# Kernel optimization log

Measured on AMD Instinct MI355X. Metric: run time of the kernel, lower is better.

Reference implementation:

```python
import jax, jax.numpy as jnp
import numpy as np

NUM_TOKENS = 131072
N_EXPERTS = 256
N_GROUP = 8
TOPK_GROUP = 4
TOP_K = 8
ROUTED_SCALING = 2.5


def setup_inputs() -> dict:
    key = jax.random.key(0)
    k1, k2 = jax.random.split(key)
    router_logits = jax.random.normal(k1, (NUM_TOKENS, N_EXPERTS), dtype=jnp.float32)
    correction_bias = jax.random.normal(k2, (N_EXPERTS,), dtype=jnp.float32) * 0.1
    return {"router_logits": router_logits, "correction_bias": correction_bias}


def reference(router_logits, correction_bias):
    T = router_logits.shape[0]
    eg = N_EXPERTS // N_GROUP  # experts per group = 32

    scores = jax.nn.sigmoid(router_logits).astype(jnp.float32)          # [T, 256]
    scores_for_choice = scores + correction_bias[None, :]                # [T, 256]

    # group score = sum of top-2 corrected scores within each group
    grp = scores_for_choice.reshape(T, N_GROUP, eg)                      # [T, 8, 32]
    top2, _ = jax.lax.top_k(grp, 2)                                      # [T, 8, 2]
    group_scores = top2.sum(axis=-1)                                     # [T, 8]

    # pick top groups, build expert-level mask
    _, group_idx = jax.lax.top_k(group_scores, TOPK_GROUP)               # [T, 4]
    rows = jnp.arange(T)[:, None]
    group_mask = jnp.zeros_like(group_scores).at[rows, group_idx].set(1.0)  # [T, 8]
    score_mask = jnp.repeat(group_mask, eg, axis=-1)                     # [T, 256]

    masked_scores = jnp.where(score_mask > 0, scores_for_choice, 0.0)
    _, topk_indices = jax.lax.top_k(masked_scores, TOP_K)                # [T, 8]

    topk_weights = jnp.take_along_axis(scores, topk_indices, axis=1)     # [T, 8]
    denom = topk_weights.sum(axis=-1, keepdims=True) + 1e-20
    topk_weights = topk_weights / denom * ROUTED_SCALING
    return (topk_indices, topk_weights)
```

## Files before the change

kernel.cpp:

```cpp
#include <hip/hip_runtime.h>
#include <math.h>


constexpr int N_EXPERTS   = 256;
constexpr int N_GROUP     = 8;
constexpr int EG          = 32;
constexpr int TOPK_GROUP  = 4;
constexpr int TOP_K       = 8;
constexpr int BLOCK       = 256;

__device__ __forceinline__ void insert8(float (&lv)[8], float (&li)[8], float v, float i) {
#pragma unroll
  for (int k = 0; k < 8; ++k) {
    const bool gt = v > lv[k];
    const float nv = gt ? lv[k] : v;
    const float ni = gt ? li[k] : i;
    lv[k] = gt ? v : lv[k];
    li[k] = gt ? i : li[k];
    v = nv; i = ni;
  }
}

__device__ __forceinline__ bool keyGE(float va, float ia, float vb, float ib) {
  return (va > vb) || (va == vb && ia < ib);
}

__device__ __forceinline__ void takeMax(float va, float ia, float vb, float ib,
                                        float& vo, float& io) {
  const bool a = keyGE(va, ia, vb, ib);
  vo = a ? va : vb;
  io = a ? ia : ib;
}

__device__ __forceinline__ void cswap(float& va, float& ia, float& vb, float& ib) {
  const bool a = keyGE(va, ia, vb, ib);
  const float v1 = a ? va : vb, i1 = a ? ia : ib;
  const float v2 = a ? vb : va, i2 = a ? ib : ia;
  va = v1; ia = i1; vb = v2; ib = i2;
}

__device__ __forceinline__ void merge8(const float (&Av)[8], const float (&Ai)[8],
                                       const float (&Bv)[8], const float (&Bi)[8],
                                       float (&Rv)[8], float (&Ri)[8]) {
#pragma unroll
  for (int i = 0; i < 8; ++i) takeMax(Av[i], Ai[i], Bv[7 - i], Bi[7 - i], Rv[i], Ri[i]);
#pragma unroll
  for (int i = 0; i < 4; ++i) cswap(Rv[i], Ri[i], Rv[i + 4], Ri[i + 4]);
  cswap(Rv[0], Ri[0], Rv[2], Ri[2]);
  cswap(Rv[1], Ri[1], Rv[3], Ri[3]);
  cswap(Rv[4], Ri[4], Rv[6], Ri[6]);
  cswap(Rv[5], Ri[5], Rv[7], Ri[7]);
  cswap(Rv[0], Ri[0], Rv[1], Ri[1]);
  cswap(Rv[2], Ri[2], Rv[3], Ri[3]);
  cswap(Rv[4], Ri[4], Rv[5], Ri[5]);
  cswap(Rv[6], Ri[6], Rv[7], Ri[7]);
}

__global__ __launch_bounds__(256, 2) void deepseek_topk_router_lds(
    const float* __restrict__ logits,
    const float* __restrict__ bias,
    float* __restrict__ out,
    int T) {
  __shared__ float gsbuf[BLOCK];
  __shared__ float exv[8 * BLOCK];
  __shared__ float exi[8 * BLOCK];

  const int tid = threadIdx.x;
  const int id  = blockIdx.x * BLOCK + tid;
  const int t   = id >> 3;
  const int q   = id & 7;

  const float4* row4 =
      reinterpret_cast<const float4*>(logits + (size_t)t * N_EXPERTS + q * EG);
  const float4* b4 = reinterpret_cast<const float4*>(bias + q * EG);

  float lv[8], li[8];
#pragma unroll
  for (int k = 0; k < 8; ++k) { lv[k] = -INFINITY; li[k] = 0.0f; }

#pragma unroll
  for (int u = 0; u < 8; ++u) {
    const float4 x = row4[u];
    const float4 bb = b4[u];
    const float xs[4] = {x.x, x.y, x.z, x.w};
    const float bs[4] = {bb.x, bb.y, bb.z, bb.w};
#pragma unroll
    for (int e = 0; e < 4; ++e) {
      const int idx = q * EG + u * 4 + e;
      const float s = 1.0f / (1.0f + expf(-xs[e]));
      const float c = s + bs[e];
      insert8(lv, li, c, (float)idx);
    }
  }

  const float gs = lv[0] + lv[1];
  gsbuf[tid] = gs;
  __syncthreads();
  const int cbase = tid & ~7;
  int rank = 0;
#pragma unroll
  for (int h = 0; h < N_GROUP; ++h) {
    const float other = gsbuf[cbase + h];
    rank += ((other > gs) || (other == gs && h < q)) ? 1 : 0;
  }
  const bool sel = (rank < TOPK_GROUP);
#pragma unroll
  for (int k = 0; k < 8; ++k) lv[k] = sel ? lv[k] : 0.0f;

  float pv[8], pi[8], rv[8], ri[8];
#pragma unroll
  for (int d = 1; d <= 4; d <<= 1) {
    __syncthreads();
#pragma unroll
    for (int k = 0; k < 8; ++k) {
      exv[k * BLOCK + tid] = lv[k];
      exi[k * BLOCK + tid] = li[k];
    }
    __syncthreads();
    const int p = tid ^ d;
#pragma unroll
    for (int k = 0; k < 8; ++k) {
      pv[k] = exv[k * BLOCK + p];
      pi[k] = exi[k * BLOCK + p];
    }
    merge8(lv, li, pv, pi, rv, ri);
#pragma unroll
    for (int k = 0; k < 8; ++k) { lv[k] = rv[k]; li[k] = ri[k]; }
  }

  float sv[8];
  float sum = 0.0f;
#pragma unroll
  for (int k = 0; k < TOP_K; ++k) {
    const int idf = (int)li[k];
    sv[k] = lv[k] - bias[idf];
    sum += sv[k];
  }
  const float scale = 2.5f / (sum + 1e-20f);

  if (q < 4) {
    float4 vout;
    if (q == 0)      vout = make_float4(li[0], li[1], li[2], li[3]);
    else if (q == 1) vout = make_float4(li[4], li[5], li[6], li[7]);
    else if (q == 2) vout = make_float4(sv[0] * scale, sv[1] * scale,
                                        sv[2] * scale, sv[3] * scale);
    else             vout = make_float4(sv[4] * scale, sv[5] * scale,
                                        sv[6] * scale, sv[7] * scale);
    const size_t half = (q < 2) ? 0 : (size_t)T * TOP_K;
    const int    sub  = q & 1;
    float4* dst = reinterpret_cast<float4*>(out + half) + (size_t)t * 2 + sub;
    *dst = vout;
  }
}

extern "C" void kernel_launch(void* const* d_in, const int* in_sizes, int n_in,
                              void* d_out, int out_size, void* d_ws, size_t ws_size,
                              hipStream_t stream) {
  const float* logits = (const float*)d_in[0];
  const float* bias   = (const float*)d_in[1];
  float* out = (float*)d_out;
  const int T = in_sizes[0] / N_EXPERTS;
  const long threads = (long)T * N_GROUP;
  const int blocks = (int)((threads + BLOCK - 1) / BLOCK);
  deepseek_topk_router_lds<<<blocks, BLOCK, 0, stream>>>(logits, bias, out, T);
}
```

Baseline: 217.8 us.

## Replace insertion top-8 and butterfly exchange with sort-merge and single LDS gather

The per-group top-8 is now built by sorting 8-element chunks with an odd-even network and merging them, replacing 32 serial insertions. After one barrier, each thread computes the four selected group indices directly and gathers those groups' sorted lists from LDS with vector loads, then merges them. This removes the three-round butterfly exchange and its six extra barriers. Launch bounds now request 4 blocks per CU. The tradeoffs are more redundant merge work per thread and higher register pressure, plus possible changes in tie-breaking order.

```diff
diff --git a/kernel.cpp b/kernel.cpp
--- a/kernel.cpp
+++ b/kernel.cpp
@@ -2,22 +2,25 @@
 #include <math.h>
 
 
-constexpr int N_EXPERTS   = 256;
-constexpr int N_GROUP     = 8;
-constexpr int EG          = 32;
-constexpr int TOPK_GROUP  = 4;
-constexpr int TOP_K       = 8;
-constexpr int BLOCK       = 256;
-
-__device__ __forceinline__ void insert8(float (&lv)[8], float (&li)[8], float v, float i) {
-#pragma unroll
-  for (int k = 0; k < 8; ++k) {
-    const bool gt = v > lv[k];
-    const float nv = gt ? lv[k] : v;
-    const float ni = gt ? li[k] : i;
-    lv[k] = gt ? v : lv[k];
-    li[k] = gt ? i : li[k];
-    v = nv; i = ni;
+constexpr int N_EXPERTS  = 256;
+constexpr int N_GROUP    = 8;
+constexpr int EG         = 32;
+constexpr int TOPK_GROUP = 4;
+constexpr int TOP_K      = 8;
+constexpr int BLOCK      = 256;
+
+__device__ __forceinline__ void sort8_stable(float (&v)[8], float (&i)[8]) {
+#pragma unroll
+  for (int r = 0; r < 8; ++r) {
+#pragma unroll
+    for (int k = (r & 1); k + 1 < 8; k += 2) {
+      const bool sw = v[k + 1] > v[k];
+      const float tv = sw ? v[k + 1] : v[k];
+      const float bv = sw ? v[k]     : v[k + 1];
+      const float ti = sw ? i[k + 1] : i[k];
+      const float bi = sw ? i[k]     : i[k + 1];
+      v[k] = tv; v[k + 1] = bv; i[k] = ti; i[k + 1] = bi;
+    }
   }
 }
 
@@ -25,45 +28,44 @@
   return (va > vb) || (va == vb && ia < ib);
 }
 
-__device__ __forceinline__ void takeMax(float va, float ia, float vb, float ib,
-                                        float& vo, float& io) {
-  const bool a = keyGE(va, ia, vb, ib);
-  vo = a ? va : vb;
-  io = a ? ia : ib;
-}
-
-__device__ __forceinline__ void cswap(float& va, float& ia, float& vb, float& ib) {
+__device__ __forceinline__ void cswapKey(float& va, float& ia, float& vb, float& ib) {
   const bool a = keyGE(va, ia, vb, ib);
   const float v1 = a ? va : vb, i1 = a ? ia : ib;
   const float v2 = a ? vb : va, i2 = a ? ib : ia;
   va = v1; ia = i1; vb = v2; ib = i2;
 }
 
-__device__ __forceinline__ void merge8(const float (&Av)[8], const float (&Ai)[8],
-                                       const float (&Bv)[8], const float (&Bi)[8],
-                                       float (&Rv)[8], float (&Ri)[8]) {
-#pragma unroll
-  for (int i = 0; i < 8; ++i) takeMax(Av[i], Ai[i], Bv[7 - i], Bi[7 - i], Rv[i], Ri[i]);
-#pragma unroll
-  for (int i = 0; i < 4; ++i) cswap(Rv[i], Ri[i], Rv[i + 4], Ri[i + 4]);
-  cswap(Rv[0], Ri[0], Rv[2], Ri[2]);
-  cswap(Rv[1], Ri[1], Rv[3], Ri[3]);
-  cswap(Rv[4], Ri[4], Rv[6], Ri[6]);
-  cswap(Rv[5], Ri[5], Rv[7], Ri[7]);
-  cswap(Rv[0], Ri[0], Rv[1], Ri[1]);
-  cswap(Rv[2], Ri[2], Rv[3], Ri[3]);
-  cswap(Rv[4], Ri[4], Rv[5], Ri[5]);
-  cswap(Rv[6], Ri[6], Rv[7], Ri[7]);
-}
-
-__global__ __launch_bounds__(256, 2) void deepseek_topk_router_lds(
+__device__ __forceinline__ void merge8AB(float (&Av)[8], float (&Ai)[8],
+                                         const float (&Bv)[8], const float (&Bi)[8]) {
+  float Rv[8], Ri[8];
+#pragma unroll
+  for (int i = 0; i < 8; ++i) {
+    const bool a = (Av[i] >= Bv[7 - i]);
+    Rv[i] = a ? Av[i] : Bv[7 - i];
+    Ri[i] = a ? Ai[i] : Bi[7 - i];
+  }
+#pragma unroll
+  for (int i = 0; i < 4; ++i) cswapKey(Rv[i], Ri[i], Rv[i + 4], Ri[i + 4]);
+  cswapKey(Rv[0], Ri[0], Rv[2], Ri[2]);
+  cswapKey(Rv[1], Ri[1], Rv[3], Ri[3]);
+  cswapKey(Rv[4], Ri[4], Rv[6], Ri[6]);
+  cswapKey(Rv[5], Ri[5], Rv[7], Ri[7]);
+  cswapKey(Rv[0], Ri[0], Rv[1], Ri[1]);
+  cswapKey(Rv[2], Ri[2], Rv[3], Ri[3]);
+  cswapKey(Rv[4], Ri[4], Rv[5], Ri[5]);
+  cswapKey(Rv[6], Ri[6], Rv[7], Ri[7]);
+#pragma unroll
+  for (int i = 0; i < 8; ++i) { Av[i] = Rv[i]; Ai[i] = Ri[i]; }
+}
+
+__global__ __launch_bounds__(256, 4) void deepseek_topk_router_r6(
     const float* __restrict__ logits,
     const float* __restrict__ bias,
     float* __restrict__ out,
     int T) {
-  __shared__ float gsbuf[BLOCK];
-  __shared__ float exv[8 * BLOCK];
-  __shared__ float exi[8 * BLOCK];
+  __shared__ float gsb[BLOCK];
+  __shared__ __align__(16) float exv[BLOCK * 8];
+  __shared__ __align__(16) float exi[BLOCK * 8];
 
   const int tid = threadIdx.x;
   const int id  = blockIdx.x * BLOCK + tid;
@@ -73,75 +75,113 @@
   const float4* row4 =
       reinterpret_cast<const float4*>(logits + (size_t)t * N_EXPERTS + q * EG);
   const float4* b4 = reinterpret_cast<const float4*>(bias + q * EG);
-
-  float lv[8], li[8];
-#pragma unroll
-  for (int k = 0; k < 8; ++k) { lv[k] = -INFINITY; li[k] = 0.0f; }
-
-#pragma unroll
-  for (int u = 0; u < 8; ++u) {
-    const float4 x = row4[u];
-    const float4 bb = b4[u];
-    const float xs[4] = {x.x, x.y, x.z, x.w};
-    const float bs[4] = {bb.x, bb.y, bb.z, bb.w};
-#pragma unroll
-    for (int e = 0; e < 4; ++e) {
-      const int idx = q * EG + u * 4 + e;
-      const float s = 1.0f / (1.0f + expf(-xs[e]));
-      const float c = s + bs[e];
-      insert8(lv, li, c, (float)idx);
+  const float basef = (float)(q * EG);
+
+  float Tv[8], Ti[8];
+  {
+    const float4 x0 = row4[0], x1 = row4[1];
+    const float4 c0 = b4[0],   c1 = b4[1];
+    const float xs[8] = {x0.x, x0.y, x0.z, x0.w, x1.x, x1.y, x1.z, x1.w};
+    const float bs[8] = {c0.x, c0.y, c0.z, c0.w, c1.x, c1.y, c1.z, c1.w};
+#pragma unroll
+    for (int j = 0; j < 8; ++j) {
+      Tv[j] = 1.0f / (1.0f + expf(-xs[j])) + bs[j];
+      Ti[j] = basef + (float)j;
     }
-  }
-
-  const float gs = lv[0] + lv[1];
-  gsbuf[tid] = gs;
+    sort8_stable(Tv, Ti);
+  }
+#pragma unroll
+  for (int c = 1; c < 4; ++c) {
+    float Cv[8], Ci[8];
+    const float4 x0 = row4[2 * c], x1 = row4[2 * c + 1];
+    const float4 c0 = b4[2 * c],   c1 = b4[2 * c + 1];
+    const float xs[8] = {x0.x, x0.y, x0.z, x0.w, x1.x, x1.y, x1.z, x1.w};
+    const float bs[8] = {c0.x, c0.y, c0.z, c0.w, c1.x, c1.y, c1.z, c1.w};
+#pragma unroll
+    for (int j = 0; j < 8; ++j) {
+      Cv[j] = 1.0f / (1.0f + expf(-xs[j])) + bs[j];
+      Ci[j] = basef + (float)(c * 8 + j);
+    }
+    sort8_stable(Cv, Ci);
+    merge8AB(Tv, Ti, Cv, Ci);
+  }
+
+  gsb[tid] = Tv[0] + Tv[1];
+#pragma unroll
+  for (int k = 0; k < 8; ++k) {
+    exv[tid * 8 + k] = Tv[k];
+    exi[tid * 8 + k] = Ti[k];
+  }
   __syncthreads();
-  const int cbase = tid & ~7;
-  int rank = 0;
+
+  const int cb = tid & ~7;
+  float g[N_GROUP];
+#pragma unroll
+  for (int h = 0; h < N_GROUP; ++h) g[h] = gsb[cb + h];
+
+  int s0 = 0, s1 = 0, s2 = 0, s3 = 0;
+  int cnt = 0;
 #pragma unroll
   for (int h = 0; h < N_GROUP; ++h) {
-    const float other = gsbuf[cbase + h];
-    rank += ((other > gs) || (other == gs && h < q)) ? 1 : 0;
-  }
-  const bool sel = (rank < TOPK_GROUP);
-#pragma unroll
-  for (int k = 0; k < 8; ++k) lv[k] = sel ? lv[k] : 0.0f;
-
-  float pv[8], pi[8], rv[8], ri[8];
-#pragma unroll
-  for (int d = 1; d <= 4; d <<= 1) {
-    __syncthreads();
-#pragma unroll
-    for (int k = 0; k < 8; ++k) {
-      exv[k * BLOCK + tid] = lv[k];
-      exi[k * BLOCK + tid] = li[k];
-    }
-    __syncthreads();
-    const int p = tid ^ d;
-#pragma unroll
-    for (int k = 0; k < 8; ++k) {
-      pv[k] = exv[k * BLOCK + p];
-      pi[k] = exi[k * BLOCK + p];
-    }
-    merge8(lv, li, pv, pi, rv, ri);
-#pragma unroll
-    for (int k = 0; k < 8; ++k) { lv[k] = rv[k]; li[k] = ri[k]; }
-  }
+    int rank = 0;
+#pragma unroll
+    for (int m = 0; m < N_GROUP; ++m)
+      rank += (m < h) ? (g[m] >= g[h] ? 1 : 0) : (g[m] > g[h] ? 1 : 0);
+    const bool pick = (rank < TOPK_GROUP);
+    s0 = (pick && cnt == 0) ? h : s0;
+    s1 = (pick && cnt == 1) ? h : s1;
+    s2 = (pick && cnt == 2) ? h : s2;
+    s3 = (pick && cnt == 3) ? h : s3;
+    cnt += pick ? 1 : 0;
+  }
+
+  float Mv[8], Mi[8], Bv[8], Bi[8], Nv[8], Ni[8];
+  {
+    const float4* pv = reinterpret_cast<const float4*>(&exv[(cb + s0) * 8]);
+    const float4* pi = reinterpret_cast<const float4*>(&exi[(cb + s0) * 8]);
+    const float4 a = pv[0], b = pv[1], c = pi[0], d = pi[1];
+    Mv[0]=a.x; Mv[1]=a.y; Mv[2]=a.z; Mv[3]=a.w; Mv[4]=b.x; Mv[5]=b.y; Mv[6]=b.z; Mv[7]=b.w;
+    Mi[0]=c.x; Mi[1]=c.y; Mi[2]=c.z; Mi[3]=c.w; Mi[4]=d.x; Mi[5]=d.y; Mi[6]=d.z; Mi[7]=d.w;
+  }
+  {
+    const float4* pv = reinterpret_cast<const float4*>(&exv[(cb + s1) * 8]);
+    const float4* pi = reinterpret_cast<const float4*>(&exi[(cb + s1) * 8]);
+    const float4 a = pv[0], b = pv[1], c = pi[0], d = pi[1];
+    Bv[0]=a.x; Bv[1]=a.y; Bv[2]=a.z; Bv[3]=a.w; Bv[4]=b.x; Bv[5]=b.y; Bv[6]=b.z; Bv[7]=b.w;
+    Bi[0]=c.x; Bi[1]=c.y; Bi[2]=c.z; Bi[3]=c.w; Bi[4]=d.x; Bi[5]=d.y; Bi[6]=d.z; Bi[7]=d.w;
+  }
+  merge8AB(Mv, Mi, Bv, Bi);
+  {
+    const float4* pv = reinterpret_cast<const float4*>(&exv[(cb + s2) * 8]);
+    const float4* pi = reinterpret_cast<const float4*>(&exi[(cb + s2) * 8]);
+    const float4 a = pv[0], b = pv[1], c = pi[0], d = pi[1];
+    Bv[0]=a.x; Bv[1]=a.y; Bv[2]=a.z; Bv[3]=a.w; Bv[4]=b.x; Bv[5]=b.y; Bv[6]=b.z; Bv[7]=b.w;
+    Bi[0]=c.x; Bi[1]=c.y; Bi[2]=c.z; Bi[3]=c.w; Bi[4]=d.x; Bi[5]=d.y; Bi[6]=d.z; Bi[7]=d.w;
+  }
+  {
+    const float4* pv = reinterpret_cast<const float4*>(&exv[(cb + s3) * 8]);
+    const float4* pi = reinterpret_cast<const float4*>(&exi[(cb + s3) * 8]);
+    const float4 a = pv[0], b = pv[1], c = pi[0], d = pi[1];
+    Nv[0]=a.x; Nv[1]=a.y; Nv[2]=a.z; Nv[3]=a.w; Nv[4]=b.x; Nv[5]=b.y; Nv[6]=b.z; Nv[7]=b.w;
+    Ni[0]=c.x; Ni[1]=c.y; Ni[2]=c.z; Ni[3]=c.w; Ni[4]=d.x; Ni[5]=d.y; Ni[6]=d.z; Ni[7]=d.w;
+  }
+  merge8AB(Bv, Bi, Nv, Ni);
+  merge8AB(Mv, Mi, Bv, Bi);
 
   float sv[8];
   float sum = 0.0f;
 #pragma unroll
   for (int k = 0; k < TOP_K; ++k) {
-    const int idf = (int)li[k];
-    sv[k] = lv[k] - bias[idf];
+    const int idf = (int)Mi[k];
+    sv[k] = Mv[k] - bias[idf];
     sum += sv[k];
   }
   const float scale = 2.5f / (sum + 1e-20f);
 
   if (q < 4) {
     float4 vout;
-    if (q == 0)      vout = make_float4(li[0], li[1], li[2], li[3]);
-    else if (q == 1) vout = make_float4(li[4], li[5], li[6], li[7]);
+    if (q == 0)      vout = make_float4(Mi[0], Mi[1], Mi[2], Mi[3]);
+    else if (q == 1) vout = make_float4(Mi[4], Mi[5], Mi[6], Mi[7]);
     else if (q == 2) vout = make_float4(sv[0] * scale, sv[1] * scale,
                                         sv[2] * scale, sv[3] * scale);
     else             vout = make_float4(sv[4] * scale, sv[5] * scale,
@@ -162,5 +202,5 @@
   const int T = in_sizes[0] / N_EXPERTS;
   const long threads = (long)T * N_GROUP;
   const int blocks = (int)((threads + BLOCK - 1) / BLOCK);
-  deepseek_topk_router_lds<<<blocks, BLOCK, 0, stream>>>(logits, bias, out, T);
-}
+  deepseek_topk_router_r6<<<blocks, BLOCK, 0, stream>>>(logits, bias, out, T);
+}
```

Measured after the change: 263.3 us. +20.9%, slower.
